# Kernel optimization log

Hardware: AMD Instinct MI355X
Metric: run time of the kernel (lower is better)

Reference implementation:

```python
import jax, jax.numpy as jnp
import numpy as np

K = 8           # neighbor_num
H = 8           # n_heads
DH = 64         # dim_single_head


def setup_inputs() -> dict:
    key = jax.random.key(0)
    ks = jax.random.split(key, 6)
    B, N, D = 2, 8192, 256
    inner = H * DH  # 512
    x = jax.random.normal(ks[0], (B, N, D), jnp.float32)
    center_pos3d = jax.random.normal(ks[1], (B, N, 3), jnp.float32)
    Wq = jax.random.normal(ks[2], (D, inner), jnp.float32) * 0.02
    Wkv = jax.random.normal(ks[3], (D, 2 * inner), jnp.float32) * 0.02
    Wout = jax.random.normal(ks[4], (inner, D), jnp.float32) * 0.02
    bout = jnp.zeros((D,), jnp.float32)
    return {"x": x, "center_pos3d": center_pos3d, "Wq": Wq, "Wkv": Wkv,
            "Wout": Wout, "bout": bout}


def _knn_idx(pos, k):
    # pos: [B,N,3] -> indices of k nearest neighbors per point, [B,N,k]
    sq = jnp.sum(pos * pos, axis=-1)                      # [B,N]
    d2 = sq[:, :, None] + sq[:, None, :] - 2.0 * jnp.einsum('bnc,bmc->bnm', pos, pos)
    _, idx = jax.lax.top_k(-d2, k)                        # smallest distances
    return idx


def reference(x, center_pos3d, Wq, Wkv, Wout, bout):
    B, N, D = x.shape
    inner = H * DH
    scale = DH ** -0.5

    idx = _knn_idx(center_pos3d, K)                       # [B,N,K] int32
    # grouping_operation: gather neighbor features -> [B,N,K,D]
    knn_x = jax.vmap(lambda xb, ib: xb[ib])(x, idx)

    q = (x @ Wq).reshape(B, N, H, DH)                     # [B,N,H,DH]
    kv = knn_x @ Wkv                                      # [B,N,K,2*inner]
    k_, v_ = jnp.split(kv, 2, axis=-1)
    k_ = k_.reshape(B, N, K, H, DH)
    v_ = v_.reshape(B, N, K, H, DH)

    dots = jnp.einsum('bnhd,bnkhd->bnhk', q, k_) * scale  # [B,N,H,K]
    attn = jax.nn.softmax(dots, axis=-1)
    out = jnp.einsum('bnhk,bnkhd->bnhd', attn, v_)        # [B,N,H,DH]
    out = out.reshape(B, N, inner)
    return out @ Wout + bout                              # dropout p=0 -> identity
```

## Files before the change

kernel.cpp:

```cpp
#include <hip/hip_runtime.h>
#include <hip/hip_bf16.h>

#define N_PTS 8192
#define KNN 8

typedef __attribute__((ext_vector_type(8))) short short8;
typedef __attribute__((ext_vector_type(4))) float float4v;
typedef unsigned long long u64;

static __device__ __forceinline__ short f2bf(float f) {
    unsigned u = __float_as_uint(f);
    unsigned r = (u + 0x7FFFu + ((u >> 16) & 1u)) >> 16;
    return (short)r;
}
static __device__ __forceinline__ float bf2f(short s) {
    return __uint_as_float(((unsigned)(unsigned short)s) << 16);
}

static __device__ __forceinline__ void ins8(u64* best, u64 x) {
#pragma unroll
    for (int j = 0; j < 8; ++j) {
        const u64 lo = x < best[j] ? x : best[j];
        const u64 hi = x < best[j] ? best[j] : x;
        best[j] = lo; x = hi;
    }
}

__global__ __launch_bounds__(256) void knn_partial(const float* __restrict__ pos,
                                                   u64* __restrict__ partial)
{
    __shared__ float sx[512], sy[512], sz[512];
    __shared__ u64 buf[256][17];

    const int tid = threadIdx.x;
    const int p   = blockIdx.x & 15;
    const int qg  = blockIdx.x >> 4;
    const int batch = qg >> 5;
    const int q_in_b = (qg & 31) * 256 + tid;
    const float* bpos = pos + (long)batch * N_PTS * 3;

    if (tid < 128) {
        const float* src = bpos + (p * 512 + tid * 4) * 3;
        const float4 f0 = *(const float4*)(src);
        const float4 f1 = *(const float4*)(src + 4);
        const float4 f2 = *(const float4*)(src + 8);
        const int c0 = tid * 4;
        *(float4*)&sx[c0] = make_float4(f0.x, f0.w, f1.z, f2.y);
        *(float4*)&sy[c0] = make_float4(f0.y, f1.x, f1.w, f2.z);
        *(float4*)&sz[c0] = make_float4(f0.z, f1.y, f2.x, f2.w);
    }
    __syncthreads();

    const float qx = bpos[q_in_b * 3 + 0];
    const float qy = bpos[q_in_b * 3 + 1];
    const float qz = bpos[q_in_b * 3 + 2];

    const float4* vx = (const float4*)sx;
    const float4* vy = (const float4*)sy;
    const float4* vz = (const float4*)sz;

    float bmin[32];
#pragma unroll
    for (int j = 0; j < 32; ++j) bmin[j] = 3.0e38f;

    for (int base = 0; base < 128; base += 8) {
#pragma unroll
        for (int g = 0; g < 8; ++g) {
            const float4 cx = vx[base + g];
            const float4 cy = vy[base + g];
            const float4 cz = vz[base + g];
            { const float dx = cx.x - qx, dy = cy.x - qy, dz = cz.x - qz;
              bmin[g*4+0] = fminf(bmin[g*4+0], fmaf(dx, dx, fmaf(dy, dy, dz*dz))); }
            { const float dx = cx.y - qx, dy = cy.y - qy, dz = cz.y - qz;
              bmin[g*4+1] = fminf(bmin[g*4+1], fmaf(dx, dx, fmaf(dy, dy, dz*dz))); }
            { const float dx = cx.z - qx, dy = cy.z - qy, dz = cz.z - qz;
              bmin[g*4+2] = fminf(bmin[g*4+2], fmaf(dx, dx, fmaf(dy, dy, dz*dz))); }
            { const float dx = cx.w - qx, dy = cy.w - qy, dz = cz.w - qz;
              bmin[g*4+3] = fminf(bmin[g*4+3], fmaf(dx, dx, fmaf(dy, dy, dz*dz))); }
        }
    }

    float t8[8];
#pragma unroll
    for (int j = 0; j < 8; ++j) t8[j] = 3.0e38f;
#pragma unroll
    for (int i = 0; i < 32; ++i) {
        float x = bmin[i];
#pragma unroll
        for (int j = 0; j < 8; ++j) {
            const float lo = fminf(t8[j], x);
            const float hi = fmaxf(t8[j], x);
            t8[j] = lo; x = hi;
        }
    }
    const float t = t8[7];

    int cnt = 0;
    for (int base = 0; base < 128; ++base) {
        const float4 cx = vx[base];
        const float4 cy = vy[base];
        const float4 cz = vz[base];
#pragma unroll
        for (int j = 0; j < 4; ++j) {
            const float ccx = j == 0 ? cx.x : j == 1 ? cx.y : j == 2 ? cx.z : cx.w;
            const float ccy = j == 0 ? cy.x : j == 1 ? cy.y : j == 2 ? cy.z : cy.w;
            const float ccz = j == 0 ? cz.x : j == 1 ? cz.y : j == 2 ? cz.z : cz.w;
            const float dx = ccx - qx, dy = ccy - qy, dz = ccz - qz;
            const float d2 = fmaf(dx, dx, fmaf(dy, dy, dz * dz));
            if (d2 <= t) {
                buf[tid][cnt < 16 ? cnt : 16] =
                    ((u64)__float_as_uint(d2) << 32)
                    | (unsigned)(p * 512 + base * 4 + j);
                ++cnt;
            }
        }
    }

    u64 best[8];
#pragma unroll
    for (int j = 0; j < 8; ++j) best[j] = ~0ULL;

    if (cnt <= 16) {
        for (int u = 0; u < cnt; ++u) {
            u64 x = buf[tid][u];
            ins8(best, x);
        }
    } else {
        for (int i = 0; i < 512; ++i) {
            const float dx = sx[i] - qx, dy = sy[i] - qy, dz = sz[i] - qz;
            const float d2 = fmaf(dx, dx, fmaf(dy, dy, dz * dz));
            u64 x = ((u64)__float_as_uint(d2) << 32) | (unsigned)(p * 512 + i);
            if (x < best[7]) ins8(best, x);
        }
    }

    const long qglob = (long)batch * N_PTS + q_in_b;
#pragma unroll
    for (int j = 0; j < 8; ++j)
        partial[(long)(p * 8 + j) * 16384 + qglob] = best[j];
}

__global__ __launch_bounds__(256) void knn_merge(const u64* __restrict__ partial,
                                                 int* __restrict__ idxo)
{
    const int q = blockIdx.x * 256 + threadIdx.x;
    u64 best[8];
#pragma unroll
    for (int j = 0; j < 8; ++j) best[j] = ~0ULL;
    for (int s = 0; s < 128; ++s) {
        u64 x = partial[(long)s * 16384 + q];
        if (x < best[7]) ins8(best, x);
    }
#pragma unroll
    for (int j = 0; j < 8; ++j)
        idxo[(long)q * 8 + j] = (int)(best[j] & 0xFFFFFFFFu);
}

__global__ __launch_bounds__(256) void conv_all(const float* __restrict__ x,
                                                const float* __restrict__ Wq,
                                                const float* __restrict__ Wkv,
                                                const float* __restrict__ Wout,
                                                short* __restrict__ xb,
                                                short* __restrict__ wqkvt,
                                                short* __restrict__ woutt)
{
    const int bid = blockIdx.x;
    const int tid = threadIdx.x;
    if (bid < 2048) {
        const int i = bid * 256 + tid;
        const float4 a = ((const float4*)x)[i * 2];
        const float4 b = ((const float4*)x)[i * 2 + 1];
        short8 w = {f2bf(a.x), f2bf(a.y), f2bf(a.z), f2bf(a.w),
                    f2bf(b.x), f2bf(b.y), f2bf(b.z), f2bf(b.w)};
        ((short8*)xb)[i] = w;
    } else if (bid < 2560) {
        const int o = (bid - 2048) * 256 + tid;
        const int n = o >> 8, k = o & 255;
        wqkvt[o] = f2bf(Wq[(long)k * 512 + n]);
    } else if (bid < 3584) {
        const int o = (bid - 2560) * 256 + tid;
        const int n = o >> 8, k = o & 255;
        wqkvt[131072 + o] = f2bf(Wkv[(long)k * 1024 + n]);
    } else {
        const int o = (bid - 3584) * 256 + tid;
        const int n = o >> 9, k = o & 511;
        woutt[o] = f2bf(Wout[(long)k * 256 + n]);
    }
}

__global__ __launch_bounds__(256) void gemm_qkv(const short* __restrict__ A,
                                                const short* __restrict__ Bt,
                                                short* __restrict__ qall,
                                                short* __restrict__ kvall)
{
    __shared__ short As[128][40];
    __shared__ short Bs[128][40];

    const int tid  = threadIdx.x;
    const int lane = tid & 63;
    const int wv   = tid >> 6;
    const int quad = lane >> 4;
    const int l15  = lane & 15;
    const int m0 = blockIdx.y * 128;
    const int n0 = blockIdx.x * 128;
    const int mh = (wv & 1) * 64, nh = (wv >> 1) * 64;

    const int srow  = tid >> 1;
    const int shalf = (tid & 1) * 16;
    const int Kd = 256;

    float4v acc[4][4];
#pragma unroll
    for (int i = 0; i < 4; ++i)
#pragma unroll
        for (int j = 0; j < 4; ++j) acc[i][j] = (float4v)(0.f);

    for (int k0 = 0; k0 < Kd; k0 += 32) {
        const short8* asrc = (const short8*)(A + (long)(m0 + srow) * Kd + k0 + shalf);
        const short8* bsrc = (const short8*)(Bt + (long)(n0 + srow) * Kd + k0 + shalf);
        *(short8*)&As[srow][shalf]     = asrc[0];
        *(short8*)&As[srow][shalf + 8] = asrc[1];
        *(short8*)&Bs[srow][shalf]     = bsrc[0];
        *(short8*)&Bs[srow][shalf + 8] = bsrc[1];
        __syncthreads();

        short8 af[4], bfv[4];
#pragma unroll
        for (int i = 0; i < 4; ++i)
            af[i] = *(const short8*)&As[mh + i * 16 + l15][quad * 8];
#pragma unroll
        for (int j = 0; j < 4; ++j)
            bfv[j] = *(const short8*)&Bs[nh + j * 16 + l15][quad * 8];
#pragma unroll
        for (int i = 0; i < 4; ++i)
#pragma unroll
            for (int j = 0; j < 4; ++j)
                acc[i][j] = __builtin_amdgcn_mfma_f32_16x16x32_bf16(af[i], bfv[j], acc[i][j], 0, 0, 0);
        __syncthreads();
    }

    short* Cb;
    int stride, cb;
    if (n0 < 512) { Cb = qall;  stride = 512;  cb = n0; }
    else          { Cb = kvall; stride = 1024; cb = n0 - 512; }

#pragma unroll
    for (int i = 0; i < 4; ++i)
#pragma unroll
        for (int j = 0; j < 4; ++j) {
            const int col = cb + nh + j * 16 + l15;
#pragma unroll
            for (int r = 0; r < 4; ++r) {
                const int row = m0 + mh + i * 16 + quad * 4 + r;
                Cb[(long)row * stride + col] = f2bf(acc[i][j][r]);
            }
        }
}

__global__ __launch_bounds__(256) void gemm_out(const short* __restrict__ A,
                                                const short* __restrict__ Bt,
                                                const float* __restrict__ bias,
                                                float* __restrict__ C,
                                                int N, int Kd)
{
    __shared__ short As[128][40];
    __shared__ short Bs[128][40];

    const int tid  = threadIdx.x;
    const int lane = tid & 63;
    const int wv   = tid >> 6;
    const int quad = lane >> 4;
    const int l15  = lane & 15;
    const int m0 = blockIdx.y * 128;
    const int n0 = blockIdx.x * 128;
    const int mh = (wv & 1) * 64, nh = (wv >> 1) * 64;

    const int srow  = tid >> 1;
    const int shalf = (tid & 1) * 16;

    float4v acc[4][4];
#pragma unroll
    for (int i = 0; i < 4; ++i)
#pragma unroll
        for (int j = 0; j < 4; ++j) acc[i][j] = (float4v)(0.f);

    for (int k0 = 0; k0 < Kd; k0 += 32) {
        const short8* asrc = (const short8*)(A + (long)(m0 + srow) * Kd + k0 + shalf);
        const short8* bsrc = (const short8*)(Bt + (long)(n0 + srow) * Kd + k0 + shalf);
        *(short8*)&As[srow][shalf]     = asrc[0];
        *(short8*)&As[srow][shalf + 8] = asrc[1];
        *(short8*)&Bs[srow][shalf]     = bsrc[0];
        *(short8*)&Bs[srow][shalf + 8] = bsrc[1];
        __syncthreads();

        short8 af[4], bfv[4];
#pragma unroll
        for (int i = 0; i < 4; ++i)
            af[i] = *(const short8*)&As[mh + i * 16 + l15][quad * 8];
#pragma unroll
        for (int j = 0; j < 4; ++j)
            bfv[j] = *(const short8*)&Bs[nh + j * 16 + l15][quad * 8];
#pragma unroll
        for (int i = 0; i < 4; ++i)
#pragma unroll
            for (int j = 0; j < 4; ++j)
                acc[i][j] = __builtin_amdgcn_mfma_f32_16x16x32_bf16(af[i], bfv[j], acc[i][j], 0, 0, 0);
        __syncthreads();
    }

#pragma unroll
    for (int i = 0; i < 4; ++i)
#pragma unroll
        for (int j = 0; j < 4; ++j) {
            const int col = n0 + nh + j * 16 + l15;
            const float bb = bias[col];
#pragma unroll
            for (int r = 0; r < 4; ++r) {
                const int row = m0 + mh + i * 16 + quad * 4 + r;
                C[(long)row * N + col] = acc[i][j][r] + bb;
            }
        }
}

__global__ __launch_bounds__(256) void attn_kernel(const short* qall,
                                                   const short* __restrict__ kvall,
                                                   const int* __restrict__ idxp,
                                                   short* outp)
{
    __shared__ float attn_s[4][8][8];
    const int wave = threadIdx.x >> 6;
    const int lane = threadIdx.x & 63;
    const int g = blockIdx.x * 4 + wave;
    const int b = g >> 13;
    const int* myidx = idxp + (long)g * 8;

    {
        const int h = lane >> 3;
        const int k = lane & 7;
        const int j = myidx[k];
        const short8* qrow = (const short8*)(qall + (long)g * 512 + h * 64);
        const short8* krow = (const short8*)(kvall + ((long)(b * N_PTS + j)) * 1024 + h * 64);

        float dot = 0.f;
#pragma unroll
        for (int c = 0; c < 8; ++c) {
            const short8 qv = qrow[c];
            const short8 kv = krow[c];
#pragma unroll
            for (int e = 0; e < 8; ++e)
                dot = fmaf(bf2f(qv[e]), bf2f(kv[e]), dot);
        }
        dot *= 0.125f;

        float m = dot;
#pragma unroll
        for (int off = 1; off < 8; off <<= 1)
            m = fmaxf(m, __shfl_xor(m, off, 8));
        const float e = __expf(dot - m);
        float ssum = e;
#pragma unroll
        for (int off = 1; off < 8; off <<= 1)
            ssum += __shfl_xor(ssum, off, 8);
        attn_s[wave][h][k] = e / ssum;
    }
    __syncthreads();

    const int d8 = lane * 8;
    const int h2 = lane >> 3;
    float o[8] = {0.f, 0.f, 0.f, 0.f, 0.f, 0.f, 0.f, 0.f};
#pragma unroll
    for (int kk = 0; kk < 8; ++kk) {
        const int jj = myidx[kk];
        const float w = attn_s[wave][h2][kk];
        const short8 v = *(const short8*)(kvall + ((long)(b * N_PTS + jj)) * 1024 + 512 + d8);
#pragma unroll
        for (int e = 0; e < 8; ++e)
            o[e] = fmaf(w, bf2f(v[e]), o[e]);
    }
    short8 ov = {f2bf(o[0]), f2bf(o[1]), f2bf(o[2]), f2bf(o[3]),
                 f2bf(o[4]), f2bf(o[5]), f2bf(o[6]), f2bf(o[7])};
    *(short8*)(outp + (long)g * 512 + d8) = ov;
}

extern "C" void kernel_launch(void* const* d_in, const int* in_sizes, int n_in,
                              void* d_out, int out_size, void* d_ws, size_t ws_size,
                              hipStream_t stream)
{
    const float* x    = (const float*)d_in[0];
    const float* pos  = (const float*)d_in[1];
    const float* Wq   = (const float*)d_in[2];
    const float* Wkv  = (const float*)d_in[3];
    const float* Wout = (const float*)d_in[4];
    const float* bout = (const float*)d_in[5];
    float* out = (float*)d_out;

    const int M = 16384;

    char* ws = (char*)d_ws;
    int*   idxp  = (int*)ws;                          ws += 1 << 19;
    short* qall  = (short*)ws;                        ws += (long)M * 512 * 2;
    short* kvall = (short*)ws;                        ws += (long)M * 1024 * 2;
    short* xb    = (short*)ws;                        ws += (long)M * 256 * 2;
    short* wqkvt = (short*)ws;                        ws += 1536 * 256 * 2;
    short* woutt = (short*)ws;                        ws += 256 * 512 * 2;
    u64* partial = (u64*)kvall;

    conv_all<<<4096, 256, 0, stream>>>(x, Wq, Wkv, Wout, xb, wqkvt, woutt);
    knn_partial<<<1024, 256, 0, stream>>>(pos, partial);
    knn_merge<<<64, 256, 0, stream>>>(partial, idxp);
    gemm_qkv<<<dim3(12, 128), 256, 0, stream>>>(xb, wqkvt, qall, kvall);
    attn_kernel<<<M / 4, 256, 0, stream>>>(qall, kvall, idxp, qall);
    gemm_out<<<dim3(2, 128), 256, 0, stream>>>(qall, woutt, bout, out, 256, 512);
}
```

Measured before the change: 311.4 us.

## Fuse KNN partial search and QKV GEMM into one heterogeneous launch

Combines the knn_partial and gemm_qkv kernels into a single launch of 2560 blocks. Blocks are interleaved in a 2:3 pattern, so ALU-heavy KNN blocks and MFMA-heavy GEMM blocks run together on the GPU. The KNN partial buffer moves out of the aliased kvall region into its own workspace, which the concurrent GEMM writes require. The cost is 40KB of shared memory and the register footprint of the larger path for every block, which can lower occupancy.

```diff
diff --git a/kernel.cpp b/kernel.cpp
--- a/kernel.cpp
+++ b/kernel.cpp
@@ -26,118 +26,196 @@
     }
 }
 
-__global__ __launch_bounds__(256) void knn_partial(const float* __restrict__ pos,
-                                                   u64* __restrict__ partial)
-{
-    __shared__ float sx[512], sy[512], sz[512];
-    __shared__ u64 buf[256][17];
+__global__ __launch_bounds__(256) void fused_knn_qkv(const float* __restrict__ pos,
+                                                     u64* __restrict__ partial,
+                                                     const short* __restrict__ A,
+                                                     const short* __restrict__ Bt,
+                                                     short* __restrict__ qall,
+                                                     short* __restrict__ kvall)
+{
+    __shared__ char smem[40960];
 
     const int tid = threadIdx.x;
-    const int p   = blockIdx.x & 15;
-    const int qg  = blockIdx.x >> 4;
-    const int batch = qg >> 5;
-    const int q_in_b = (qg & 31) * 256 + tid;
-    const float* bpos = pos + (long)batch * N_PTS * 3;
-
-    if (tid < 128) {
-        const float* src = bpos + (p * 512 + tid * 4) * 3;
-        const float4 f0 = *(const float4*)(src);
-        const float4 f1 = *(const float4*)(src + 4);
-        const float4 f2 = *(const float4*)(src + 8);
-        const int c0 = tid * 4;
-        *(float4*)&sx[c0] = make_float4(f0.x, f0.w, f1.z, f2.y);
-        *(float4*)&sy[c0] = make_float4(f0.y, f1.x, f1.w, f2.z);
-        *(float4*)&sz[c0] = make_float4(f0.z, f1.y, f2.x, f2.w);
-    }
-    __syncthreads();
-
-    const float qx = bpos[q_in_b * 3 + 0];
-    const float qy = bpos[q_in_b * 3 + 1];
-    const float qz = bpos[q_in_b * 3 + 2];
-
-    const float4* vx = (const float4*)sx;
-    const float4* vy = (const float4*)sy;
-    const float4* vz = (const float4*)sz;
-
-    float bmin[32];
-#pragma unroll
-    for (int j = 0; j < 32; ++j) bmin[j] = 3.0e38f;
-
-    for (int base = 0; base < 128; base += 8) {
-#pragma unroll
-        for (int g = 0; g < 8; ++g) {
-            const float4 cx = vx[base + g];
-            const float4 cy = vy[base + g];
-            const float4 cz = vz[base + g];
-            { const float dx = cx.x - qx, dy = cy.x - qy, dz = cz.x - qz;
-              bmin[g*4+0] = fminf(bmin[g*4+0], fmaf(dx, dx, fmaf(dy, dy, dz*dz))); }
-            { const float dx = cx.y - qx, dy = cy.y - qy, dz = cz.y - qz;
-              bmin[g*4+1] = fminf(bmin[g*4+1], fmaf(dx, dx, fmaf(dy, dy, dz*dz))); }
-            { const float dx = cx.z - qx, dy = cy.z - qy, dz = cz.z - qz;
-              bmin[g*4+2] = fminf(bmin[g*4+2], fmaf(dx, dx, fmaf(dy, dy, dz*dz))); }
-            { const float dx = cx.w - qx, dy = cy.w - qy, dz = cz.w - qz;
-              bmin[g*4+3] = fminf(bmin[g*4+3], fmaf(dx, dx, fmaf(dy, dy, dz*dz))); }
-        }
-    }
-
-    float t8[8];
-#pragma unroll
-    for (int j = 0; j < 8; ++j) t8[j] = 3.0e38f;
-#pragma unroll
-    for (int i = 0; i < 32; ++i) {
-        float x = bmin[i];
-#pragma unroll
-        for (int j = 0; j < 8; ++j) {
-            const float lo = fminf(t8[j], x);
-            const float hi = fmaxf(t8[j], x);
-            t8[j] = lo; x = hi;
-        }
-    }
-    const float t = t8[7];
-
-    int cnt = 0;
-    for (int base = 0; base < 128; ++base) {
-        const float4 cx = vx[base];
-        const float4 cy = vy[base];
-        const float4 cz = vz[base];
-#pragma unroll
-        for (int j = 0; j < 4; ++j) {
-            const float ccx = j == 0 ? cx.x : j == 1 ? cx.y : j == 2 ? cx.z : cx.w;
-            const float ccy = j == 0 ? cy.x : j == 1 ? cy.y : j == 2 ? cy.z : cy.w;
-            const float ccz = j == 0 ? cz.x : j == 1 ? cz.y : j == 2 ? cz.z : cz.w;
-            const float dx = ccx - qx, dy = ccy - qy, dz = ccz - qz;
-            const float d2 = fmaf(dx, dx, fmaf(dy, dy, dz * dz));
-            if (d2 <= t) {
-                buf[tid][cnt < 16 ? cnt : 16] =
-                    ((u64)__float_as_uint(d2) << 32)
-                    | (unsigned)(p * 512 + base * 4 + j);
-                ++cnt;
-            }
-        }
-    }
-
-    u64 best[8];
-#pragma unroll
-    for (int j = 0; j < 8; ++j) best[j] = ~0ULL;
-
-    if (cnt <= 16) {
-        for (int u = 0; u < cnt; ++u) {
-            u64 x = buf[tid][u];
-            ins8(best, x);
-        }
+    const int g5 = blockIdx.x / 5;
+    const int r5 = blockIdx.x % 5;
+
+    if (r5 < 2) {
+        const int kb = g5 * 2 + r5;
+        float* sx = (float*)smem;
+        float* sy = sx + 512;
+        float* sz = sy + 512;
+        u64* buf = (u64*)(smem + 6144);
+
+        const int p   = kb & 15;
+        const int qg  = kb >> 4;
+        const int batch = qg >> 5;
+        const int q_in_b = (qg & 31) * 256 + tid;
+        const float* bpos = pos + (long)batch * N_PTS * 3;
+
+        if (tid < 128) {
+            const float* src = bpos + (p * 512 + tid * 4) * 3;
+            const float4 f0 = *(const float4*)(src);
+            const float4 f1 = *(const float4*)(src + 4);
+            const float4 f2 = *(const float4*)(src + 8);
+            const int c0 = tid * 4;
+            *(float4*)&sx[c0] = make_float4(f0.x, f0.w, f1.z, f2.y);
+            *(float4*)&sy[c0] = make_float4(f0.y, f1.x, f1.w, f2.z);
+            *(float4*)&sz[c0] = make_float4(f0.z, f1.y, f2.x, f2.w);
+        }
+        __syncthreads();
+
+        const float qx = bpos[q_in_b * 3 + 0];
+        const float qy = bpos[q_in_b * 3 + 1];
+        const float qz = bpos[q_in_b * 3 + 2];
+
+        const float4* vx = (const float4*)sx;
+        const float4* vy = (const float4*)sy;
+        const float4* vz = (const float4*)sz;
+
+        float bmin[32];
+#pragma unroll
+        for (int j = 0; j < 32; ++j) bmin[j] = 3.0e38f;
+
+        for (int base = 0; base < 128; base += 8) {
+#pragma unroll
+            for (int g = 0; g < 8; ++g) {
+                const float4 cx = vx[base + g];
+                const float4 cy = vy[base + g];
+                const float4 cz = vz[base + g];
+                { const float dx = cx.x - qx, dy = cy.x - qy, dz = cz.x - qz;
+                  bmin[g*4+0] = fminf(bmin[g*4+0], fmaf(dx, dx, fmaf(dy, dy, dz*dz))); }
+                { const float dx = cx.y - qx, dy = cy.y - qy, dz = cz.y - qz;
+                  bmin[g*4+1] = fminf(bmin[g*4+1], fmaf(dx, dx, fmaf(dy, dy, dz*dz))); }
+                { const float dx = cx.z - qx, dy = cy.z - qy, dz = cz.z - qz;
+                  bmin[g*4+2] = fminf(bmin[g*4+2], fmaf(dx, dx, fmaf(dy, dy, dz*dz))); }
+                { const float dx = cx.w - qx, dy = cy.w - qy, dz = cz.w - qz;
+                  bmin[g*4+3] = fminf(bmin[g*4+3], fmaf(dx, dx, fmaf(dy, dy, dz*dz))); }
+            }
+        }
+
+        float t8[8];
+#pragma unroll
+        for (int j = 0; j < 8; ++j) t8[j] = 3.0e38f;
+#pragma unroll
+        for (int i = 0; i < 32; ++i) {
+            float x = bmin[i];
+#pragma unroll
+            for (int j = 0; j < 8; ++j) {
+                const float lo = fminf(t8[j], x);
+                const float hi = fmaxf(t8[j], x);
+                t8[j] = lo; x = hi;
+            }
+        }
+        const float t = t8[7];
+
+        int cnt = 0;
+        for (int base = 0; base < 128; ++base) {
+            const float4 cx = vx[base];
+            const float4 cy = vy[base];
+            const float4 cz = vz[base];
+#pragma unroll
+            for (int j = 0; j < 4; ++j) {
+                const float ccx = j == 0 ? cx.x : j == 1 ? cx.y : j == 2 ? cx.z : cx.w;
+                const float ccy = j == 0 ? cy.x : j == 1 ? cy.y : j == 2 ? cy.z : cy.w;
+                const float ccz = j == 0 ? cz.x : j == 1 ? cz.y : j == 2 ? cz.z : cz.w;
+                const float dx = ccx - qx, dy = ccy - qy, dz = ccz - qz;
+                const float d2 = fmaf(dx, dx, fmaf(dy, dy, dz * dz));
+                if (d2 <= t) {
+                    buf[tid * 17 + (cnt < 16 ? cnt : 16)] =
+                        ((u64)__float_as_uint(d2) << 32)
+                        | (unsigned)(p * 512 + base * 4 + j);
+                    ++cnt;
+                }
+            }
+        }
+
+        u64 best[8];
+#pragma unroll
+        for (int j = 0; j < 8; ++j) best[j] = ~0ULL;
+
+        if (cnt <= 16) {
+            for (int u = 0; u < cnt; ++u) ins8(best, buf[tid * 17 + u]);
+        } else {
+            for (int i = 0; i < 512; ++i) {
+                const float dx = sx[i] - qx, dy = sy[i] - qy, dz = sz[i] - qz;
+                const float d2 = fmaf(dx, dx, fmaf(dy, dy, dz * dz));
+                u64 x = ((u64)__float_as_uint(d2) << 32) | (unsigned)(p * 512 + i);
+                if (x < best[7]) ins8(best, x);
+            }
+        }
+
+        const long qglob = (long)batch * N_PTS + q_in_b;
+#pragma unroll
+        for (int j = 0; j < 8; ++j)
+            partial[(long)(p * 8 + j) * 16384 + qglob] = best[j];
+
     } else {
-        for (int i = 0; i < 512; ++i) {
-            const float dx = sx[i] - qx, dy = sy[i] - qy, dz = sz[i] - qz;
-            const float d2 = fmaf(dx, dx, fmaf(dy, dy, dz * dz));
-            u64 x = ((u64)__float_as_uint(d2) << 32) | (unsigned)(p * 512 + i);
-            if (x < best[7]) ins8(best, x);
-        }
-    }
-
-    const long qglob = (long)batch * N_PTS + q_in_b;
-#pragma unroll
-    for (int j = 0; j < 8; ++j)
-        partial[(long)(p * 8 + j) * 16384 + qglob] = best[j];
+        const int id = g5 * 3 + (r5 - 2);
+        const int bx = id % 12;
+        const int by = id / 12;
+
+        short (*As)[40] = (short(*)[40])smem;
+        short (*Bs)[40] = (short(*)[40])(smem + 10240);
+
+        const int lane = tid & 63;
+        const int wv   = tid >> 6;
+        const int quad = lane >> 4;
+        const int l15  = lane & 15;
+        const int m0 = by * 128;
+        const int n0 = bx * 128;
+        const int mh = (wv & 1) * 64, nh = (wv >> 1) * 64;
+
+        const int srow  = tid >> 1;
+        const int shalf = (tid & 1) * 16;
+        const int Kd = 256;
+
+        float4v acc[4][4];
+#pragma unroll
+        for (int i = 0; i < 4; ++i)
+#pragma unroll
+            for (int j = 0; j < 4; ++j) acc[i][j] = (float4v)(0.f);
+
+        for (int k0 = 0; k0 < Kd; k0 += 32) {
+            const short8* asrc = (const short8*)(A + (long)(m0 + srow) * Kd + k0 + shalf);
+            const short8* bsrc = (const short8*)(Bt + (long)(n0 + srow) * Kd + k0 + shalf);
+            *(short8*)&As[srow][shalf]     = asrc[0];
+            *(short8*)&As[srow][shalf + 8] = asrc[1];
+            *(short8*)&Bs[srow][shalf]     = bsrc[0];
+            *(short8*)&Bs[srow][shalf + 8] = bsrc[1];
+            __syncthreads();
+
+            short8 af[4], bfv[4];
+#pragma unroll
+            for (int i = 0; i < 4; ++i)
+                af[i] = *(const short8*)&As[mh + i * 16 + l15][quad * 8];
+#pragma unroll
+            for (int j = 0; j < 4; ++j)
+                bfv[j] = *(const short8*)&Bs[nh + j * 16 + l15][quad * 8];
+#pragma unroll
+            for (int i = 0; i < 4; ++i)
+#pragma unroll
+                for (int j = 0; j < 4; ++j)
+                    acc[i][j] = __builtin_amdgcn_mfma_f32_16x16x32_bf16(af[i], bfv[j], acc[i][j], 0, 0, 0);
+            __syncthreads();
+        }
+
+        short* Cb;
+        int stride, cb;
+        if (n0 < 512) { Cb = qall;  stride = 512;  cb = n0; }
+        else          { Cb = kvall; stride = 1024; cb = n0 - 512; }
+
+#pragma unroll
+        for (int i = 0; i < 4; ++i)
+#pragma unroll
+            for (int j = 0; j < 4; ++j) {
+                const int col = cb + nh + j * 16 + l15;
+#pragma unroll
+                for (int r = 0; r < 4; ++r) {
+                    const int row = m0 + mh + i * 16 + quad * 4 + r;
+                    Cb[(long)row * stride + col] = f2bf(acc[i][j][r]);
+                }
+            }
+    }
 }
 
 __global__ __launch_bounds__(256) void knn_merge(const u64* __restrict__ partial,
@@ -188,10 +266,11 @@
     }
 }
 
-__global__ __launch_bounds__(256) void gemm_qkv(const short* __restrict__ A,
+__global__ __launch_bounds__(256) void gemm_out(const short* __restrict__ A,
                                                 const short* __restrict__ Bt,
-                                                short* __restrict__ qall,
-                                                short* __restrict__ kvall)
+                                                const float* __restrict__ bias,
+                                                float* __restrict__ C,
+                                                int N, int Kd)
 {
     __shared__ short As[128][40];
     __shared__ short Bs[128][40];
@@ -207,7 +286,6 @@
 
     const int srow  = tid >> 1;
     const int shalf = (tid & 1) * 16;
-    const int Kd = 256;
 
     float4v acc[4][4];
 #pragma unroll
@@ -239,75 +317,6 @@
         __syncthreads();
     }
 
-    short* Cb;
-    int stride, cb;
-    if (n0 < 512) { Cb = qall;  stride = 512;  cb = n0; }
-    else          { Cb = kvall; stride = 1024; cb = n0 - 512; }
-
-#pragma unroll
-    for (int i = 0; i < 4; ++i)
-#pragma unroll
-        for (int j = 0; j < 4; ++j) {
-            const int col = cb + nh + j * 16 + l15;
-#pragma unroll
-            for (int r = 0; r < 4; ++r) {
-                const int row = m0 + mh + i * 16 + quad * 4 + r;
-                Cb[(long)row * stride + col] = f2bf(acc[i][j][r]);
-            }
-        }
-}
-
-__global__ __launch_bounds__(256) void gemm_out(const short* __restrict__ A,
-                                                const short* __restrict__ Bt,
-                                                const float* __restrict__ bias,
-                                                float* __restrict__ C,
-                                                int N, int Kd)
-{
-    __shared__ short As[128][40];
-    __shared__ short Bs[128][40];
-
-    const int tid  = threadIdx.x;
-    const int lane = tid & 63;
-    const int wv   = tid >> 6;
-    const int quad = lane >> 4;
-    const int l15  = lane & 15;
-    const int m0 = blockIdx.y * 128;
-    const int n0 = blockIdx.x * 128;
-    const int mh = (wv & 1) * 64, nh = (wv >> 1) * 64;
-
-    const int srow  = tid >> 1;
-    const int shalf = (tid & 1) * 16;
-
-    float4v acc[4][4];
-#pragma unroll
-    for (int i = 0; i < 4; ++i)
-#pragma unroll
-        for (int j = 0; j < 4; ++j) acc[i][j] = (float4v)(0.f);
-
-    for (int k0 = 0; k0 < Kd; k0 += 32) {
-        const short8* asrc = (const short8*)(A + (long)(m0 + srow) * Kd + k0 + shalf);
-        const short8* bsrc = (const short8*)(Bt + (long)(n0 + srow) * Kd + k0 + shalf);
-        *(short8*)&As[srow][shalf]     = asrc[0];
-        *(short8*)&As[srow][shalf + 8] = asrc[1];
-        *(short8*)&Bs[srow][shalf]     = bsrc[0];
-        *(short8*)&Bs[srow][shalf + 8] = bsrc[1];
-        __syncthreads();
-
-        short8 af[4], bfv[4];
-#pragma unroll
-        for (int i = 0; i < 4; ++i)
-            af[i] = *(const short8*)&As[mh + i * 16 + l15][quad * 8];
-#pragma unroll
-        for (int j = 0; j < 4; ++j)
-            bfv[j] = *(const short8*)&Bs[nh + j * 16 + l15][quad * 8];
-#pragma unroll
-        for (int i = 0; i < 4; ++i)
-#pragma unroll
-            for (int j = 0; j < 4; ++j)
-                acc[i][j] = __builtin_amdgcn_mfma_f32_16x16x32_bf16(af[i], bfv[j], acc[i][j], 0, 0, 0);
-        __syncthreads();
-    }
-
 #pragma unroll
     for (int i = 0; i < 4; ++i)
 #pragma unroll
@@ -403,12 +412,11 @@
     short* xb    = (short*)ws;                        ws += (long)M * 256 * 2;
     short* wqkvt = (short*)ws;                        ws += 1536 * 256 * 2;
     short* woutt = (short*)ws;                        ws += 256 * 512 * 2;
-    u64* partial = (u64*)kvall;
+    u64*  partial = (u64*)ws;                         ws += (long)128 * 16384 * 8;
 
     conv_all<<<4096, 256, 0, stream>>>(x, Wq, Wkv, Wout, xb, wqkvt, woutt);
-    knn_partial<<<1024, 256, 0, stream>>>(pos, partial);
+    fused_knn_qkv<<<2560, 256, 0, stream>>>(pos, partial, xb, wqkvt, qall, kvall);
     knn_merge<<<64, 256, 0, stream>>>(partial, idxp);
-    gemm_qkv<<<dim3(12, 128), 256, 0, stream>>>(xb, wqkvt, qall, kvall);
     attn_kernel<<<M / 4, 256, 0, stream>>>(qall, kvall, idxp, qall);
     gemm_out<<<dim3(2, 128), 256, 0, stream>>>(qall, woutt, bout, out, 256, 512);
 }
```

New measurement: 323.1 us. +3.7%, slower.
